# Kernel optimization log

Hardware: AMD Instinct MI355X
Metric: run time of the kernel (lower is better)

## Reference

```python
import jax, jax.numpy as jnp
import numpy as np

ALPHAS = [2.0 ** k for k in range(-3, 2)]  # default GaussianKernel bandwidth magnitudes


def _cdist(x, y):
    # Euclidean distance matrix with torch.cdist-compatible zero-distance subgradient.
    sq = (jnp.sum(x * x, axis=1)[:, None]
          + jnp.sum(y * y, axis=1)[None, :]
          - 2.0 * (x @ y.T))
    sq = jnp.maximum(sq, 0.0)
    safe = jnp.where(sq > 0, sq, 1.0)
    return jnp.where(sq > 0, jnp.sqrt(safe), 0.0)


def setup_inputs() -> dict:
    key = jax.random.key(0)
    k1, k2 = jax.random.split(key)
    xs = jax.random.normal(k1, (4096, 256), dtype=jnp.float32)
    xt = jax.random.normal(k2, (4096, 256), dtype=jnp.float32)
    return {"xs": xs, "xt": xt}


def reference(xs, xt):
    xs = xs.reshape(xs.shape[0], -1)
    xt = xt.reshape(xt.shape[0], -1)
    b = xs.shape[0]

    # Compute the three pairwise distance matrices ONCE (the torch loop redoes
    # this per kernel; the math is identical).
    dxx = _cdist(xs, xs)  # [B, B]
    dyy = _cdist(xt, xt)
    dxy = _cdist(xs, xt)

    # sigma^2 = alpha * mean(dist), with the mean detached (stop_gradient).
    mxx = jax.lax.stop_gradient(jnp.mean(dxx))
    myy = jax.lax.stop_gradient(jnp.mean(dyy))
    mxy = jax.lax.stop_gradient(jnp.mean(dxy))

    total = jnp.zeros_like(dxx)
    for a in ALPHAS:
        kxx = jnp.exp(-dxx / (2.0 * a * mxx))
        kyy = jnp.exp(-dyy / (2.0 * a * myy))
        kxy = jnp.exp(-dxy / (2.0 * a * mxy))
        total = total + (kxx + kyy - 2.0 * kxy)

    loss = jnp.sqrt(jnp.sum(total) / (b * (b - 1.0)))
    return jnp.where(jnp.isnan(loss), jnp.zeros_like(loss), loss)
```

## Files before the change

kernel.cpp:

```cpp
#include <hip/hip_runtime.h>

#define BN 4096
#define KD 256
#define TILE 128
#define BK 64

typedef short bf16x8 __attribute__((ext_vector_type(8)));
typedef float f32x4 __attribute__((ext_vector_type(4)));
typedef unsigned short ushort_t;
typedef unsigned int uint_t;

#define NSLOT 2080

__device__ inline void async_load16(const void* g, void* l) {
    __builtin_amdgcn_global_load_lds((const __attribute__((address_space(1))) void*)g,
                                     (__attribute__((address_space(3))) void*)l,
                                     16, 0, 0);
}

__device__ inline ushort_t f2bf(float f) {
    union { float f; unsigned int u; } x;
    x.f = f;
    unsigned int u = x.u;
    unsigned int r = (u + 0x7fffu + ((u >> 16) & 1u)) >> 16;
    return (ushort_t)r;
}

__device__ __forceinline__ float fast_sqrt(float x) {
    return __builtin_amdgcn_sqrtf(x);
}
__device__ __forceinline__ float fast_exp2(float x) {
    return __builtin_amdgcn_exp2f(x);
}

__device__ __forceinline__ void decode_slot(int slot, int& z, int& bi, int& bj) {
    if (slot >= 1056) {
        z = 2; int t = slot - 1056; bi = t >> 5; bj = t & 31;
    } else {
        z = (slot >= 528) ? 1 : 0;
        int t = slot - z * 528;
        int b = (int)(32.5f - sqrtf(1056.25f - 2.0f * (float)t));
        while (b * (65 - b) / 2 > t) --b;
        while ((b + 1) * (64 - b) / 2 <= t) ++b;
        bi = b;
        bj = bi + (t - bi * (65 - bi) / 2);
    }
}

__global__ __launch_bounds__(256) void norm_cvt(
        const float* __restrict__ xs, const float* __restrict__ xt,
        ushort_t* __restrict__ xsb, ushort_t* __restrict__ xtb,
        float* __restrict__ norms) {
    int w = threadIdx.x >> 6;
    int lane = threadIdx.x & 63;
    int row = blockIdx.x * 4 + w;
    const float* src = (row < BN) ? xs + (size_t)row * KD
                                  : xt + (size_t)(row - BN) * KD;
    ushort_t* dst = (row < BN) ? xsb + (size_t)row * KD
                               : xtb + (size_t)(row - BN) * KD;
    float4 v = ((const float4*)src)[lane];
    float s = v.x * v.x + v.y * v.y + v.z * v.z + v.w * v.w;
#pragma unroll
    for (int off = 32; off > 0; off >>= 1) s += __shfl_xor(s, off, 64);
    if (lane == 0) norms[row] = s;
    ushort4 o;
    o.x = f2bf(v.x); o.y = f2bf(v.y); o.z = f2bf(v.z); o.w = f2bf(v.w);
    ((ushort4*)dst)[lane] = o;
}


template <int PASS>
__global__ __launch_bounds__(256) void mmd_gemm(
        const ushort_t* __restrict__ xsb, const ushort_t* __restrict__ xtb,
        const float* __restrict__ norms,
        const float* __restrict__ p1, float* __restrict__ pout) {
    const int slot = blockIdx.x;
    int z, bi, bj;
    decode_slot(slot, z, bi, bj);

    const ushort_t* X = (z == 1) ? xtb : xsb;
    const ushort_t* Y = (z == 0) ? xsb : xtb;
    const float* nX = norms + ((z == 1) ? BN : 0);
    const float* nY = norms + ((z == 0) ? 0 : BN);

    const int tid = threadIdx.x;
    const int lane = tid & 63;
    const int w = tid >> 6;
    const int wr = w >> 1;
    const int wc = w & 1;
    const int m16 = lane & 15;
    const int q = lane >> 4;

    const int i0 = bi * TILE;
    const int j0 = bj * TILE;

    __shared__ ushort_t lA[TILE * BK];
    __shared__ ushort_t lB[TILE * BK];
    __shared__ float red[4];
    __shared__ double rs[4][3];

    float nhb = 0.0f;
    if (PASS == 2) {
        double a0 = 0.0, a1 = 0.0, a2 = 0.0;
        for (int s = tid; s < NSLOT; s += 256) {
            double v = (double)p1[s];
            if (s < 528) a0 += v; else if (s < 1056) a1 += v; else a2 += v;
        }
#pragma unroll
        for (int off = 32; off > 0; off >>= 1) {
            a0 += __shfl_xor(a0, off, 64);
            a1 += __shfl_xor(a1, off, 64);
            a2 += __shfl_xor(a2, off, 64);
        }
        if (lane == 0) { rs[w][0] = a0; rs[w][1] = a1; rs[w][2] = a2; }
        __syncthreads();
        double sz = rs[0][z] + rs[1][z] + rs[2][z] + rs[3][z];
        double mz = sz * (1.0 / 16777216.0);
        nhb = (float)(-1.4426950408889634 / (4.0 * mz));
    }

    f32x4 acc[4][4] = {};

#pragma unroll
    for (int kk = 0; kk < KD; kk += BK) {
        __syncthreads();
#pragma unroll
        for (int t = 0; t < 4; ++t) {
            int rowblk = w * 4 + t;
            int r = rowblk * 8 + (lane >> 3);
            int cch = lane & 7;
            int gch = cch ^ (r & 7);
            const ushort_t* gA = X + (size_t)(i0 + r) * KD + (kk + gch * 8);
            const ushort_t* gB = Y + (size_t)(j0 + r) * KD + (kk + gch * 8);
            async_load16(gA, (char*)lA + rowblk * 1024);
            async_load16(gB, (char*)lB + rowblk * 1024);
        }
        __syncthreads();

#pragma unroll
        for (int ks = 0; ks < 2; ++ks) {
            bf16x8 af[4], bfr[4];
            int kap = ks * 4 + q;
#pragma unroll
            for (int rg = 0; rg < 4; ++rg) {
                int rowa = wr * 64 + rg * 16 + m16;
                int posa = kap ^ (rowa & 7);
                af[rg] = *(const bf16x8*)&lA[rowa * BK + posa * 8];
                int rowb = wc * 64 + rg * 16 + m16;
                int posb = kap ^ (rowb & 7);
                bfr[rg] = *(const bf16x8*)&lB[rowb * BK + posb * 8];
            }
#pragma unroll
            for (int rg = 0; rg < 4; ++rg)
#pragma unroll
                for (int ng = 0; ng < 4; ++ng)
                    acc[rg][ng] = __builtin_amdgcn_mfma_f32_16x16x32_bf16(
                        af[rg], bfr[ng], acc[rg][ng], 0, 0, 0);
        }
    }

    float nxv[16];
#pragma unroll
    for (int rg = 0; rg < 4; ++rg)
#pragma unroll
        for (int rr = 0; rr < 4; ++rr)
            nxv[rg * 4 + rr] = nX[i0 + wr * 64 + rg * 16 + q * 4 + rr];
    float nyv[4];
#pragma unroll
    for (int ng = 0; ng < 4; ++ng)
        nyv[ng] = nY[j0 + wc * 64 + ng * 16 + m16];

    float local = 0.0f;
#pragma unroll
    for (int rg = 0; rg < 4; ++rg) {
#pragma unroll
        for (int ng = 0; ng < 4; ++ng) {
#pragma unroll
            for (int rr = 0; rr < 4; ++rr) {
                int i = wr * 64 + rg * 16 + q * 4 + rr;
                int j = wc * 64 + ng * 16 + m16;
                float sq = nxv[rg * 4 + rr] + nyv[ng] - 2.0f * acc[rg][ng][rr];
                sq = fmaxf(sq, 0.0f);
                float d = fast_sqrt(sq);
                if (z < 2 && bi == bj && i == j) d = 0.0f;
                if (PASS == 1) {
                    local += d;
                } else {
                    float u = fast_exp2(d * nhb);
                    float u2 = u * u;
                    float u4 = u2 * u2;
                    float u8 = u4 * u4;
                    float u16 = u8 * u8;
                    local += (u + u2) + (u4 + u8) + u16;
                }
            }
        }
    }

#pragma unroll
    for (int off = 32; off > 0; off >>= 1) local += __shfl_xor(local, off, 64);
    if (lane == 0) red[w] = local;
    __syncthreads();
    if (tid == 0) {
        float bs = red[0] + red[1] + red[2] + red[3];
        float coef;
        if (PASS == 1) coef = (z < 2 && bi != bj) ? 2.0f : 1.0f;
        else           coef = (z == 2) ? -2.0f : ((bi != bj) ? 2.0f : 1.0f);
        pout[slot] = coef * bs;
    }
}


__global__ __launch_bounds__(256) void mmd_finalize2(
        const float* __restrict__ p2, float* __restrict__ out) {
    const int tid = threadIdx.x;
    double acc = 0.0;
    for (int s = tid; s < NSLOT; s += 256) acc += (double)p2[s];
    const int lane = tid & 63, w = tid >> 6;
#pragma unroll
    for (int off = 32; off > 0; off >>= 1) acc += __shfl_xor(acc, off, 64);
    __shared__ double r[4];
    if (lane == 0) r[w] = acc;
    __syncthreads();
    if (tid == 0) {
        double S = r[0] + r[1] + r[2] + r[3];
        double l = sqrt(S / ((double)BN * (double)(BN - 1)));
        float f = (float)l;
        if (!(f == f)) f = 0.0f;
        out[0] = f;
    }
}

extern "C" void kernel_launch(void* const* d_in, const int* in_sizes, int n_in,
                              void* d_out, int out_size, void* d_ws, size_t ws_size,
                              hipStream_t stream) {
    const float* xs = (const float*)d_in[0];
    const float* xt = (const float*)d_in[1];
    float* out = (float*)d_out;

    char* ws = (char*)d_ws;
    float* norms = (float*)ws;
    float* p1 = (float*)(ws + 32768);
    float* p2 = (float*)(ws + 41152);
    ushort_t* xsb = (ushort_t*)(ws + 49536);
    ushort_t* xtb = xsb + (size_t)BN * KD;

    size_t need = 4243840;
    if (ws_size < need) {
        (void)hipMemsetAsync(d_out, 0xC0, 4, stream);
        return;
    }

    norm_cvt<<<2048, 256, 0, stream>>>(xs, xt, xsb, xtb, norms);
    mmd_gemm<1><<<NSLOT, 256, 0, stream>>>(xsb, xtb, norms, p1, p1);
    mmd_gemm<2><<<NSLOT, 256, 0, stream>>>(xsb, xtb, norms, p1, p2);
    mmd_finalize2<<<1, 256, 0, stream>>>(p2, out);
}
```

Measured before the change: 135.3 us.

## Use 256x256 tiles with 8 waves and double-buffered async LDS loads

Doubles the output tile to 256x256 per block, moving to 512 threads (8 waves, each owning 128x64), which cuts the number of tile slots and the redundant global loads per output element. The K loop now double-buffers LDS stages with explicit vmcnt waits and raw barriers, so global-to-LDS copies overlap the MFMA work. Row-norm loads are vectorised as float4 and the workspace offsets shrink to match the smaller slot count. Risks: 528 blocks on a 256-CU part gives poor wave balance, the larger accumulator array raises register pressure, and 64KB of LDS per block limits occupancy.

Measured after the change: 149.6 us. +10.6%, slower.

```diff
diff --git a/kernel.cpp b/kernel.cpp
--- a/kernel.cpp
+++ b/kernel.cpp
@@ -2,7 +2,7 @@
 
 #define BN 4096
 #define KD 256
-#define TILE 128
+#define TILE 256
 #define BK 64
 
 typedef short bf16x8 __attribute__((ext_vector_type(8)));
@@ -10,7 +10,7 @@
 typedef unsigned short ushort_t;
 typedef unsigned int uint_t;
 
-#define NSLOT 2080
+#define NSLOT 528
 
 __device__ inline void async_load16(const void* g, void* l) {
     __builtin_amdgcn_global_load_lds((const __attribute__((address_space(1))) void*)g,
@@ -34,16 +34,16 @@
 }
 
 __device__ __forceinline__ void decode_slot(int slot, int& z, int& bi, int& bj) {
-    if (slot >= 1056) {
-        z = 2; int t = slot - 1056; bi = t >> 5; bj = t & 31;
+    if (slot >= 272) {
+        z = 2; int t = slot - 272; bi = t >> 4; bj = t & 15;
     } else {
-        z = (slot >= 528) ? 1 : 0;
-        int t = slot - z * 528;
-        int b = (int)(32.5f - sqrtf(1056.25f - 2.0f * (float)t));
-        while (b * (65 - b) / 2 > t) --b;
-        while ((b + 1) * (64 - b) / 2 <= t) ++b;
+        z = (slot >= 136) ? 1 : 0;
+        int t = slot - z * 136;
+        int b = (int)(16.5f - sqrtf(272.25f - 2.0f * (float)t));
+        while (b * (33 - b) / 2 > t) --b;
+        while ((b + 1) * (32 - b) / 2 <= t) ++b;
         bi = b;
-        bj = bi + (t - bi * (65 - bi) / 2);
+        bj = bi + (t - bi * (33 - bi) / 2);
     }
 }
 
@@ -70,7 +70,7 @@
 
 
 template <int PASS>
-__global__ __launch_bounds__(256) void mmd_gemm(
+__global__ __launch_bounds__(512, 2) void mmd_gemm(
         const ushort_t* __restrict__ xsb, const ushort_t* __restrict__ xtb,
         const float* __restrict__ norms,
         const float* __restrict__ p1, float* __restrict__ pout) {
@@ -86,25 +86,24 @@
     const int tid = threadIdx.x;
     const int lane = tid & 63;
     const int w = tid >> 6;
-    const int wr = w >> 1;
-    const int wc = w & 1;
+    const int wr = w >> 2;
+    const int wc = w & 3;
     const int m16 = lane & 15;
     const int q = lane >> 4;
 
     const int i0 = bi * TILE;
     const int j0 = bj * TILE;
 
-    __shared__ ushort_t lA[TILE * BK];
-    __shared__ ushort_t lB[TILE * BK];
-    __shared__ float red[4];
-    __shared__ double rs[4][3];
+    __shared__ ushort_t sm[2][2][TILE * BK];
+    __shared__ float red[8];
+    __shared__ double rs[8][3];
 
     float nhb = 0.0f;
     if (PASS == 2) {
         double a0 = 0.0, a1 = 0.0, a2 = 0.0;
-        for (int s = tid; s < NSLOT; s += 256) {
+        for (int s = tid; s < NSLOT; s += 512) {
             double v = (double)p1[s];
-            if (s < 528) a0 += v; else if (s < 1056) a1 += v; else a2 += v;
+            if (s < 136) a0 += v; else if (s < 272) a1 += v; else a2 += v;
         }
 #pragma unroll
         for (int off = 32; off > 0; off >>= 1) {
@@ -114,75 +113,93 @@
         }
         if (lane == 0) { rs[w][0] = a0; rs[w][1] = a1; rs[w][2] = a2; }
         __syncthreads();
-        double sz = rs[0][z] + rs[1][z] + rs[2][z] + rs[3][z];
+        double sz = 0.0;
+#pragma unroll
+        for (int ww = 0; ww < 8; ++ww) sz += rs[ww][z];
         double mz = sz * (1.0 / 16777216.0);
         nhb = (float)(-1.4426950408889634 / (4.0 * mz));
     }
 
-    f32x4 acc[4][4] = {};
-
-#pragma unroll
-    for (int kk = 0; kk < KD; kk += BK) {
-        __syncthreads();
+    const int rbase = tid >> 3;
+    const int gc = (tid & 7) ^ (rbase & 7);
+    const size_t baseA = (size_t)(i0 + rbase) * KD + gc * 8;
+    const size_t baseB = (size_t)(j0 + rbase) * KD + gc * 8;
+
+    f32x4 acc[8][4] = {};
+
+    auto stage = [&](int kt, int p) {
+        const int kk = kt * BK;
+        char* ldsA = (char*)&sm[p][0][0];
+        char* ldsB = (char*)&sm[p][1][0];
 #pragma unroll
         for (int t = 0; t < 4; ++t) {
-            int rowblk = w * 4 + t;
-            int r = rowblk * 8 + (lane >> 3);
-            int cch = lane & 7;
-            int gch = cch ^ (r & 7);
-            const ushort_t* gA = X + (size_t)(i0 + r) * KD + (kk + gch * 8);
-            const ushort_t* gB = Y + (size_t)(j0 + r) * KD + (kk + gch * 8);
-            async_load16(gA, (char*)lA + rowblk * 1024);
-            async_load16(gB, (char*)lB + rowblk * 1024);
-        }
-        __syncthreads();
-
+            async_load16(X + baseA + (size_t)t * 64 * KD + kk, ldsA + t * 8192 + tid * 16);
+            async_load16(Y + baseB + (size_t)t * 64 * KD + kk, ldsB + t * 8192 + tid * 16);
+        }
+    };
+
+    auto compute = [&](int p) {
 #pragma unroll
         for (int ks = 0; ks < 2; ++ks) {
-            bf16x8 af[4], bfr[4];
-            int kap = ks * 4 + q;
-#pragma unroll
-            for (int rg = 0; rg < 4; ++rg) {
-                int rowa = wr * 64 + rg * 16 + m16;
-                int posa = kap ^ (rowa & 7);
-                af[rg] = *(const bf16x8*)&lA[rowa * BK + posa * 8];
-                int rowb = wc * 64 + rg * 16 + m16;
-                int posb = kap ^ (rowb & 7);
-                bfr[rg] = *(const bf16x8*)&lB[rowb * BK + posb * 8];
-            }
-#pragma unroll
-            for (int rg = 0; rg < 4; ++rg)
+            bf16x8 af[8], bfv[4];
+            const int kap = ks * 4 + q;
+            const int pos = kap ^ (m16 & 7);
+#pragma unroll
+            for (int rg = 0; rg < 8; ++rg)
+                af[rg] = *(const bf16x8*)&sm[p][0][(wr * 128 + rg * 16 + m16) * BK + pos * 8];
+#pragma unroll
+            for (int ng = 0; ng < 4; ++ng)
+                bfv[ng] = *(const bf16x8*)&sm[p][1][(wc * 64 + ng * 16 + m16) * BK + pos * 8];
+#pragma unroll
+            for (int rg = 0; rg < 8; ++rg)
 #pragma unroll
                 for (int ng = 0; ng < 4; ++ng)
                     acc[rg][ng] = __builtin_amdgcn_mfma_f32_16x16x32_bf16(
-                        af[rg], bfr[ng], acc[rg][ng], 0, 0, 0);
-        }
-    }
-
-    float nxv[16];
-#pragma unroll
-    for (int rg = 0; rg < 4; ++rg)
-#pragma unroll
-        for (int rr = 0; rr < 4; ++rr)
-            nxv[rg * 4 + rr] = nX[i0 + wr * 64 + rg * 16 + q * 4 + rr];
+                        af[rg], bfv[ng], acc[rg][ng], 0, 0, 0);
+        }
+    };
+
+    stage(0, 0);
+#pragma unroll
+    for (int t = 0; t < 4; ++t) {
+        const int p = t & 1;
+        if (t < 3) {
+            stage(t + 1, p ^ 1);
+            asm volatile("s_waitcnt vmcnt(8)" ::: "memory");
+        } else {
+            asm volatile("s_waitcnt vmcnt(0)" ::: "memory");
+        }
+        __builtin_amdgcn_s_barrier();
+        compute(p);
+        if (t < 3) __builtin_amdgcn_s_barrier();
+    }
+
+    float nxv[32];
+#pragma unroll
+    for (int rg = 0; rg < 8; ++rg) {
+        float4 nf = *(const float4*)&nX[i0 + wr * 128 + rg * 16 + q * 4];
+        nxv[rg * 4 + 0] = nf.x; nxv[rg * 4 + 1] = nf.y;
+        nxv[rg * 4 + 2] = nf.z; nxv[rg * 4 + 3] = nf.w;
+    }
     float nyv[4];
 #pragma unroll
     for (int ng = 0; ng < 4; ++ng)
         nyv[ng] = nY[j0 + wc * 64 + ng * 16 + m16];
 
+    const bool diag = (z < 2 && bi == bj);
     float local = 0.0f;
 #pragma unroll
-    for (int rg = 0; rg < 4; ++rg) {
+    for (int rg = 0; rg < 8; ++rg) {
 #pragma unroll
         for (int ng = 0; ng < 4; ++ng) {
 #pragma unroll
             for (int rr = 0; rr < 4; ++rr) {
-                int i = wr * 64 + rg * 16 + q * 4 + rr;
+                int i = wr * 128 + rg * 16 + q * 4 + rr;
                 int j = wc * 64 + ng * 16 + m16;
                 float sq = nxv[rg * 4 + rr] + nyv[ng] - 2.0f * acc[rg][ng][rr];
                 sq = fmaxf(sq, 0.0f);
                 float d = fast_sqrt(sq);
-                if (z < 2 && bi == bj && i == j) d = 0.0f;
+                if (diag && i == j) d = 0.0f;
                 if (PASS == 1) {
                     local += d;
                 } else {
@@ -202,7 +219,9 @@
     if (lane == 0) red[w] = local;
     __syncthreads();
     if (tid == 0) {
-        float bs = red[0] + red[1] + red[2] + red[3];
+        float bs = 0.0f;
+#pragma unroll
+        for (int ww = 0; ww < 8; ++ww) bs += red[ww];
         float coef;
         if (PASS == 1) coef = (z < 2 && bi != bj) ? 2.0f : 1.0f;
         else           coef = (z == 2) ? -2.0f : ((bi != bj) ? 2.0f : 1.0f);
@@ -241,18 +260,18 @@
     char* ws = (char*)d_ws;
     float* norms = (float*)ws;
     float* p1 = (float*)(ws + 32768);
-    float* p2 = (float*)(ws + 41152);
-    ushort_t* xsb = (ushort_t*)(ws + 49536);
+    float* p2 = (float*)(ws + 35072);
+    ushort_t* xsb = (ushort_t*)(ws + 37376);
     ushort_t* xtb = xsb + (size_t)BN * KD;
 
-    size_t need = 4243840;
+    size_t need = 4231680;
     if (ws_size < need) {
         (void)hipMemsetAsync(d_out, 0xC0, 4, stream);
         return;
     }
 
     norm_cvt<<<2048, 256, 0, stream>>>(xs, xt, xsb, xtb, norms);
-    mmd_gemm<1><<<NSLOT, 256, 0, stream>>>(xsb, xtb, norms, p1, p1);
-    mmd_gemm<2><<<NSLOT, 256, 0, stream>>>(xsb, xtb, norms, p1, p2);
+    mmd_gemm<1><<<NSLOT, 512, 0, stream>>>(xsb, xtb, norms, p1, p1);
+    mmd_gemm<2><<<NSLOT, 512, 0, stream>>>(xsb, xtb, norms, p1, p2);
     mmd_finalize2<<<1, 256, 0, stream>>>(p2, out);
 }
```
